# Kernel optimization log

Measured on AMD Instinct MI355X. Metric: run time of the kernel, lower is better.

The kernel has to match this reference:

```python
import jax, jax.numpy as jnp
import numpy as np

B, C, H, W = 64, 128, 56, 56
ALPHA = 0.001


def _build_inhi_mat(out_channels):
    # Circulant 0/1 band: row i has ones at columns (i-r//2 ... i+r//2) mod C,
    # exactly matching the torch double loop with modular wrap-around.
    r = out_channels // 8 + 1  # inhiRange
    i = np.arange(out_channels)[:, None]
    d = np.arange(-(r // 2), r // 2 + 1)[None, :]
    cols = (i + d) % out_channels  # [C, r]
    m = np.zeros((out_channels, out_channels), dtype=np.float32)
    m[np.repeat(i, d.shape[1], axis=1), cols] = 1.0
    return m


def setup_inputs() -> dict:
    key = jax.random.key(0)
    x = jax.random.normal(key, (B, C, H, W), dtype=jnp.float32)
    inhiMat = jnp.asarray(_build_inhi_mat(C))  # [C, C] constant buffer
    return {"x": x, "inhiMat": inhiMat}


def reference(x, inhiMat):
    b, c, h, w = x.shape
    inhiRange = c // 8 + 1
    # y = detach(x)^2 -> banded cross-channel sum (bmm with broadcast [C,C] mat)
    y = jax.lax.stop_gradient(x) ** 2
    y = y.reshape(b, c, h * w)
    y = jnp.einsum('ij,bjs->bis', inhiMat, y)  # same math as bmm with tiled inhi
    y = y.reshape(b, c, h, w)
    denom = (y * ALPHA / inhiRange + 1.0) ** 0.75
    return x / denom
```

## Files before the change

kernel.cpp:

```cpp
#include <hip/hip_runtime.h>


#define B_DIM 64
#define C_DIM 128
#define HW_DIM (56 * 56)
#define HW2 (HW_DIM / 2)
#define NCOL (B_DIM * HW2)

__device__ __forceinline__ float pow_m075(float t) {
    return __builtin_amdgcn_exp2f(-0.75f * __builtin_amdgcn_logf(t));
}

__global__ __launch_bounds__(64) void lrn_kernel(const float2* __restrict__ x,
                                                 float2* __restrict__ out) {
    const float kAlphaOverR = 0.001f / 17.0f;

    const int col = blockIdx.x * 64 + threadIdx.x;
    const int b   = col / HW2;
    const int hw2 = col - b * HW2;

    const float2* base = x + ((size_t)b * C_DIM) * HW2 + hw2;
    float2* obase      = out + ((size_t)b * C_DIM) * HW2 + hw2;

    float sx = 0.f, sy = 0.f;
#pragma unroll
    for (int d = -8; d <= 8; ++d) {
        const int ch = (d + C_DIM) & (C_DIM - 1);
        const float2 v = base[(size_t)ch * HW2];
        sx += v.x * v.x;
        sy += v.y * v.y;
    }

#pragma unroll 8
    for (int c = 0; c < C_DIM; ++c) {
        const float2 xc = base[(size_t)c * HW2];

        float2 r;
        r.x = xc.x * pow_m075(fmaf(sx, kAlphaOverR, 1.0f));
        r.y = xc.y * pow_m075(fmaf(sy, kAlphaOverR, 1.0f));
        obase[(size_t)c * HW2] = r;

        const int ci = (c + 9) & (C_DIM - 1);
        const int co = (c - 8 + C_DIM) & (C_DIM - 1);
        const float2 vin  = base[(size_t)ci * HW2];
        const float2 vout = base[(size_t)co * HW2];
        sx += vin.x * vin.x - vout.x * vout.x;
        sy += vin.y * vin.y - vout.y * vout.y;
    }
}

extern "C" void kernel_launch(void* const* d_in, const int* in_sizes, int n_in,
                              void* d_out, int out_size, void* d_ws, size_t ws_size,
                              hipStream_t stream) {
    const float2* x = (const float2*)d_in[0];
    float2* out = (float2*)d_out;

    lrn_kernel<<<NCOL / 64, 64, 0, stream>>>(x, out);
}
```

Baseline: 193.5 us.

## Split channel sweep into two segments and use scalar per-pixel threads

Each thread now handles one pixel instead of a float2 pair, and the 128-channel sliding-window sweep is split into two 64-channel segments across a second grid dimension. This raises the number of waves and in-flight memory requests to hide latency in the sequential channel loop. The cost is a duplicated 17-channel window prologue per segment and narrower per-lane loads.

```diff
diff --git a/kernel.cpp b/kernel.cpp
--- a/kernel.cpp
+++ b/kernel.cpp
@@ -4,56 +4,55 @@
 #define B_DIM 64
 #define C_DIM 128
 #define HW_DIM (56 * 56)
-#define HW2 (HW_DIM / 2)
-#define NCOL (B_DIM * HW2)
+#define NCOL (B_DIM * HW_DIM)
+#define NSEG 2
+#define SEGC (C_DIM / NSEG)
 
 __device__ __forceinline__ float pow_m075(float t) {
     return __builtin_amdgcn_exp2f(-0.75f * __builtin_amdgcn_logf(t));
 }
 
-__global__ __launch_bounds__(64) void lrn_kernel(const float2* __restrict__ x,
-                                                 float2* __restrict__ out) {
+__global__ __launch_bounds__(128) void lrn_kernel(const float* __restrict__ x,
+                                                  float* __restrict__ out) {
     const float kAlphaOverR = 0.001f / 17.0f;
 
-    const int col = blockIdx.x * 64 + threadIdx.x;
-    const int b   = col / HW2;
-    const int hw2 = col - b * HW2;
+    const int col = blockIdx.x * 128 + threadIdx.x;
+    const int b   = col / HW_DIM;
+    const int hw  = col - b * HW_DIM;
+    const int c0  = blockIdx.y * SEGC;
 
-    const float2* base = x + ((size_t)b * C_DIM) * HW2 + hw2;
-    float2* obase      = out + ((size_t)b * C_DIM) * HW2 + hw2;
+    const float* base = x + ((size_t)b * C_DIM) * HW_DIM + hw;
+    float* obase      = out + ((size_t)b * C_DIM) * HW_DIM + hw;
 
-    float sx = 0.f, sy = 0.f;
+    float s = 0.f;
 #pragma unroll
     for (int d = -8; d <= 8; ++d) {
-        const int ch = (d + C_DIM) & (C_DIM - 1);
-        const float2 v = base[(size_t)ch * HW2];
-        sx += v.x * v.x;
-        sy += v.y * v.y;
+        const int ch = (c0 + d + C_DIM) & (C_DIM - 1);
+        const float v = base[(size_t)ch * HW_DIM];
+        s += v * v;
     }
 
 #pragma unroll 8
-    for (int c = 0; c < C_DIM; ++c) {
-        const float2 xc = base[(size_t)c * HW2];
+    for (int i = 0; i < SEGC; ++i) {
+        const int c = c0 + i;
+        const float xc = base[(size_t)c * HW_DIM];
 
-        float2 r;
-        r.x = xc.x * pow_m075(fmaf(sx, kAlphaOverR, 1.0f));
-        r.y = xc.y * pow_m075(fmaf(sy, kAlphaOverR, 1.0f));
-        obase[(size_t)c * HW2] = r;
+        obase[(size_t)c * HW_DIM] = xc * pow_m075(fmaf(s, kAlphaOverR, 1.0f));
 
         const int ci = (c + 9) & (C_DIM - 1);
         const int co = (c - 8 + C_DIM) & (C_DIM - 1);
-        const float2 vin  = base[(size_t)ci * HW2];
-        const float2 vout = base[(size_t)co * HW2];
-        sx += vin.x * vin.x - vout.x * vout.x;
-        sy += vin.y * vin.y - vout.y * vout.y;
+        const float vin  = base[(size_t)ci * HW_DIM];
+        const float vout = base[(size_t)co * HW_DIM];
+        s += vin * vin - vout * vout;
     }
 }
 
 extern "C" void kernel_launch(void* const* d_in, const int* in_sizes, int n_in,
                               void* d_out, int out_size, void* d_ws, size_t ws_size,
                               hipStream_t stream) {
-    const float2* x = (const float2*)d_in[0];
-    float2* out = (float2*)d_out;
+    const float* x = (const float*)d_in[0];
+    float* out = (float*)d_out;
 
-    lrn_kernel<<<NCOL / 64, 64, 0, stream>>>(x, out);
+    dim3 grid(NCOL / 128, NSEG);
+    lrn_kernel<<<grid, 128, 0, stream>>>(x, out);
 }
```

Result: no change. 195.1 us (+0.8%).

## Keep sliding channel window in a register ring and split channels across grid

Applied to the files above, without the earlier changes.

Each thread now holds the 17 most recent channel values in a fully unrolled register ring. This removes the repeated global reloads of the center and outgoing channels, so each input is read roughly once instead of three times. The channel dimension is also split into two segments along grid.y, which doubles the number of blocks for more parallelism. The cost is a 16-channel halo reload per segment and higher register pressure from the full unroll.

```diff
diff --git a/kernel.cpp b/kernel.cpp
--- a/kernel.cpp
+++ b/kernel.cpp
@@ -5,7 +5,10 @@
 #define C_DIM 128
 #define HW_DIM (56 * 56)
 #define HW2 (HW_DIM / 2)
-#define NCOL (B_DIM * HW2)
+#define NCOL2 (B_DIM * HW2)
+#define NSEG 2
+#define SEGC (C_DIM / NSEG)
+#define RING 17
 
 __device__ __forceinline__ float pow_m075(float t) {
     return __builtin_amdgcn_exp2f(-0.75f * __builtin_amdgcn_logf(t));
@@ -18,34 +21,43 @@
     const int col = blockIdx.x * 64 + threadIdx.x;
     const int b   = col / HW2;
     const int hw2 = col - b * HW2;
+    const int c0  = blockIdx.y * SEGC;
 
     const float2* base = x + ((size_t)b * C_DIM) * HW2 + hw2;
     float2* obase      = out + ((size_t)b * C_DIM) * HW2 + hw2;
 
+    float2 r[RING];
+#pragma unroll
+    for (int d = 0; d < RING; ++d) {
+        const int ch = (c0 + d - 8 + C_DIM) & (C_DIM - 1);
+        r[d] = base[(size_t)ch * HW2];
+    }
     float sx = 0.f, sy = 0.f;
 #pragma unroll
-    for (int d = -8; d <= 8; ++d) {
-        const int ch = (d + C_DIM) & (C_DIM - 1);
-        const float2 v = base[(size_t)ch * HW2];
-        sx += v.x * v.x;
-        sy += v.y * v.y;
+    for (int d = 0; d < RING; ++d) {
+        sx += r[d].x * r[d].x;
+        sy += r[d].y * r[d].y;
     }
 
-#pragma unroll 8
-    for (int c = 0; c < C_DIM; ++c) {
-        const float2 xc = base[(size_t)c * HW2];
+#pragma unroll
+    for (int i = 0; i < SEGC; ++i) {
+        const int c = c0 + i;
+        const int slot_out = i % RING;
+        const int slot_x   = (i + 8) % RING;
+        const int ch_in    = (c + 9) & (C_DIM - 1);
 
-        float2 r;
-        r.x = xc.x * pow_m075(fmaf(sx, kAlphaOverR, 1.0f));
-        r.y = xc.y * pow_m075(fmaf(sy, kAlphaOverR, 1.0f));
-        obase[(size_t)c * HW2] = r;
+        const float2 vin = base[(size_t)ch_in * HW2];
 
-        const int ci = (c + 9) & (C_DIM - 1);
-        const int co = (c - 8 + C_DIM) & (C_DIM - 1);
-        const float2 vin  = base[(size_t)ci * HW2];
-        const float2 vout = base[(size_t)co * HW2];
+        const float2 xc = r[slot_x];
+        float2 o;
+        o.x = xc.x * pow_m075(fmaf(sx, kAlphaOverR, 1.0f));
+        o.y = xc.y * pow_m075(fmaf(sy, kAlphaOverR, 1.0f));
+        obase[(size_t)c * HW2] = o;
+
+        const float2 vout = r[slot_out];
         sx += vin.x * vin.x - vout.x * vout.x;
         sy += vin.y * vin.y - vout.y * vout.y;
+        r[slot_out] = vin;
     }
 }
 
@@ -55,5 +67,6 @@
     const float2* x = (const float2*)d_in[0];
     float2* out = (float2*)d_out;
 
-    lrn_kernel<<<NCOL / 64, 64, 0, stream>>>(x, out);
+    dim3 grid(NCOL2 / 64, NSEG);
+    lrn_kernel<<<grid, 64, 0, stream>>>(x, out);
 }
```

New measurement: 187.6 us. 3.0% less time.
